# Kernel optimization log

Measured on AMD Instinct MI355X. Metric: run time of the kernel, lower is better.

The kernel has to match this reference:

```python
import jax, jax.numpy as jnp
import numpy as np

N_HEAD = 8

def setup_inputs() -> dict:
    key = jax.random.key(0)
    ks = jax.random.split(key, 5)
    B, T, C = 2, 4096, 512
    x = jax.random.normal(ks[0], (B, T, C), dtype=jnp.float32)
    w_attn = jax.random.normal(ks[1], (3 * C, C), dtype=jnp.float32) * (1.0 / np.sqrt(C))
    b_attn = jax.random.normal(ks[2], (3 * C,), dtype=jnp.float32) * 0.02
    w_proj = jax.random.normal(ks[3], (C, C), dtype=jnp.float32) * (1.0 / np.sqrt(C))
    b_proj = jax.random.normal(ks[4], (C,), dtype=jnp.float32) * 0.02
    return {"x": x, "w_attn": w_attn, "b_attn": b_attn, "w_proj": w_proj, "b_proj": b_proj}

def reference(x, w_attn, b_attn, w_proj, b_proj):
    B, T, C = x.shape
    H = N_HEAD
    D = C // H  # head dim
    qkv = x @ w_attn.T + b_attn  # [B,T,3C]
    q, k, v = jnp.split(qkv, 3, axis=-1)
    # b t (h d) -> b h t d
    def to_heads(t):
        return t.reshape(B, T, H, D).transpose(0, 2, 1, 3)
    q, k, v = to_heads(q), to_heads(k), to_heads(v)
    scale = 1.0 / np.sqrt(D).astype(np.float32)
    att = jnp.einsum('bhqd,bhkd->bhqk', q, k) * scale  # [B,H,T,T]
    causal = jnp.tril(jnp.ones((T, T), dtype=bool))
    att = jnp.where(causal[None, None], att, jnp.float32(-jnp.inf))
    att = jax.nn.softmax(att, axis=-1)
    y = jnp.einsum('bhqk,bhkd->bhqd', att, v)  # [B,H,T,D]
    y = y.transpose(0, 2, 1, 3).reshape(B, T, C)
    return y @ w_proj.T + b_proj
```

## Files before the change

kernel.cpp:

```cpp
#include <hip/hip_runtime.h>

typedef __attribute__((ext_vector_type(8))) __bf16 bf16x8;
typedef __attribute__((ext_vector_type(4))) __bf16 bf16x4;
typedef __attribute__((ext_vector_type(4))) float f32x4;
typedef __attribute__((ext_vector_type(16))) float f32x16;
typedef __attribute__((ext_vector_type(4))) unsigned uint32x4;

#define AS1 __attribute__((address_space(1)))
#define AS3 __attribute__((address_space(3)))

#if __has_builtin(__builtin_amdgcn_exp2f)
#define EXP2(x) __builtin_amdgcn_exp2f(x)
#else
#define EXP2(x) exp2f(x)
#endif

#define QSCALE 0.18033688011112042f

#define N_X 4194304
#define N_WA 786432
#define N_WP 262144
__global__ __launch_bounds__(256) void convert_all_k(const float* __restrict__ x,
                                                     const float* __restrict__ wa,
                                                     const float* __restrict__ wp,
                                                     __bf16* __restrict__ xb,
                                                     __bf16* __restrict__ wab,
                                                     __bf16* __restrict__ wpb) {
  int i = (blockIdx.x * 256 + threadIdx.x) * 4;
  const float* src;
  __bf16* dst;
  int off;
  if (i < N_X)              { src = x;  dst = xb;  off = i; }
  else if (i < N_X + N_WA)  { src = wa; dst = wab; off = i - N_X; }
  else if (i < N_X + N_WA + N_WP) { src = wp; dst = wpb; off = i - N_X - N_WA; }
  else return;
  float4 v = *reinterpret_cast<const float4*>(src + off);
  bf16x4 o;
  o[0] = (__bf16)v.x; o[1] = (__bf16)v.y; o[2] = (__bf16)v.z; o[3] = (__bf16)v.w;
  *reinterpret_cast<bf16x4*>(dst + off) = o;
}

template <int EPI>
__global__ __launch_bounds__(256) void gemm_bt(const __bf16* __restrict__ A,
                                               const __bf16* __restrict__ Bm,
                                               const float* __restrict__ bias,
                                               void* __restrict__ outp,
                                               __bf16* __restrict__ vtout,
                                               int M, int N, int K) {
  __shared__ __bf16 a_lds[128 * 64];
  __shared__ __bf16 b_lds[128 * 64];
  const int tid = threadIdx.x;
  const int lane = tid & 63;
  const int w = tid >> 6;
  const int wm = w >> 1, wn = w & 1;
  const int ll = lane & 15, lh = lane >> 4;
  const int m0 = blockIdx.y * 128;
  const int n0 = blockIdx.x * 128;
  f32x4 acc[4][4] = {};

  for (int k0 = 0; k0 < K; k0 += 64) {
    __syncthreads();
#pragma unroll
    for (int i = 0; i < 4; ++i) {
      int ch = i * 256 + w * 64 + lane;
      int r = ch >> 3, c8 = ch & 7;
      const __bf16* ga = A + (size_t)(m0 + r) * K + k0 + c8 * 8;
      __builtin_amdgcn_global_load_lds((const AS1 void*)ga,
                                       (AS3 void*)(a_lds + (i * 256 + w * 64) * 8), 16, 0, 0);
      const __bf16* gb = Bm + (size_t)(n0 + r) * K + k0 + c8 * 8;
      __builtin_amdgcn_global_load_lds((const AS1 void*)gb,
                                       (AS3 void*)(b_lds + (i * 256 + w * 64) * 8), 16, 0, 0);
    }
    __syncthreads();
#pragma unroll
    for (int kc = 0; kc < 2; ++kc) {
      bf16x8 af[4], bfr[4];
#pragma unroll
      for (int m = 0; m < 4; ++m)
        af[m] = *reinterpret_cast<const bf16x8*>(a_lds + (wm * 64 + m * 16 + ll) * 64 + kc * 32 + lh * 8);
#pragma unroll
      for (int n = 0; n < 4; ++n)
        bfr[n] = *reinterpret_cast<const bf16x8*>(b_lds + (wn * 64 + n * 16 + ll) * 64 + kc * 32 + lh * 8);
#pragma unroll
      for (int m = 0; m < 4; ++m)
#pragma unroll
        for (int n = 0; n < 4; ++n)
          acc[m][n] = __builtin_amdgcn_mfma_f32_16x16x32_bf16(af[m], bfr[n], acc[m][n], 0, 0, 0);
    }
  }
  if (EPI == 1) {
#pragma unroll
    for (int m = 0; m < 4; ++m) {
      int gm = m0 + wm * 64 + m * 16 + lh * 4;
#pragma unroll
      for (int n = 0; n < 4; ++n) {
        int gn = n0 + wn * 64 + n * 16 + ll;
        float bs = bias[gn];
#pragma unroll
        for (int r = 0; r < 4; ++r)
          ((float*)outp)[(size_t)(gm + r) * N + gn] = acc[m][n][r] + bs;
      }
    }
  } else if (n0 < 1024) {
    __syncthreads();
    __bf16* tb = (w < 2 ? a_lds : b_lds) + (w & 1) * 4096;
    const float sc = (n0 < 512) ? (float)QSCALE : 1.0f;
#pragma unroll
    for (int m = 0; m < 4; ++m)
#pragma unroll
      for (int n = 0; n < 4; ++n) {
        float bs = bias[n0 + wn * 64 + n * 16 + ll];
#pragma unroll
        for (int r = 0; r < 4; ++r)
          tb[(m * 16 + lh * 4 + r) * 64 + n * 16 + ll] = (__bf16)((acc[m][n][r] + bs) * sc);
      }
    const int rsub = lane >> 3, csub = (lane & 7) * 8;
#pragma unroll
    for (int i = 0; i < 8; ++i) {
      bf16x8 vv = *reinterpret_cast<const bf16x8*>(tb + (i * 8 + rsub) * 64 + csub);
      *reinterpret_cast<bf16x8*>((__bf16*)outp +
          (size_t)(m0 + wm * 64 + i * 8 + rsub) * N + n0 + wn * 64 + csub) = vv;
    }
  } else {
#pragma unroll
    for (int m = 0; m < 4; ++m) {
      int gm = m0 + wm * 64 + m * 16 + lh * 4;
#pragma unroll
      for (int n = 0; n < 4; ++n) {
        int gn = n0 + wn * 64 + n * 16 + ll;
        float bs = bias[gn];
        bf16x4 pk;
#pragma unroll
        for (int r = 0; r < 4; ++r) pk[r] = (__bf16)(acc[m][n][r] + bs);
        *reinterpret_cast<bf16x4*>(vtout + ((size_t)((gm >> 12) * 512 + (gn - 1024))) * 4096 + (gm & 4095)) = pk;
      }
    }
  }
}

struct Tbl { unsigned short t[204]; };
constexpr Tbl build_tbl() {
  Tbl T{};
  int sizes[204] = {};
  int n = 0;
  for (int p = 0; p < 2; ++p)
    for (int qx = 0; qx < 32; ++qx) {
      int total = 2 * qx + 2;
      int nch = (total + 11) / 12;
      int cum = 0;
      for (int q = 0; q < qx; ++q) cum += (2 * q + 13) / 12;
      for (int c = 0; c < nch; ++c) {
        int sz = total - 12 * c; if (sz > 12) sz = 12;
        T.t[n] = (unsigned short)(qx | (c << 5) | (p << 8) | ((cum + c) << 9));
        sizes[n] = sz;
        ++n;
      }
    }
  for (int i = 1; i < n; ++i) {
    unsigned short tv = T.t[i]; int sv = sizes[i];
    int j = i - 1;
    while (j >= 0 && sizes[j] < sv) { T.t[j + 1] = T.t[j]; sizes[j + 1] = sizes[j]; --j; }
    T.t[j + 1] = tv; sizes[j + 1] = sv;
  }
  return T;
}
__device__ __constant__ Tbl g_tbl = build_tbl();

__device__ inline unsigned cvtpk(float lo, float hi_) {
  unsigned r;
  asm("v_cvt_pk_bf16_f32 %0, %1, %2" : "=v"(r) : "v"(lo), "v"(hi_));
  return r;
}

__global__ __launch_bounds__(256, 4) void attn_k(const __bf16* __restrict__ qkv,
                                                 const __bf16* __restrict__ vt,
                                                 __bf16* __restrict__ opart,
                                                 float* __restrict__ lpart,
                                                 __bf16* __restrict__ y) {
  __shared__ __bf16 k_lds[2][64 * 64];
  __shared__ __bf16 v_lds[2][64 * 64];
  const int tid = threadIdx.x, lane = tid & 63, w = tid >> 6;
  const int hi = lane >> 5, q31 = lane & 31;
  const int swz = q31 & 7;

  const int bid = (int)blockIdx.x;
  const int e = g_tbl.t[bid >> 3];
  const int qx = e & 31, c = (e >> 5) & 7, p = (e >> 8) & 1, j = e >> 9;
  const int bh = (bid & 7) * 2 + p;
  const int pslot = bh * 102 + j;
  const int b = bh >> 3, h = bh & 7;
  const int q0 = qx * 128;
  const int qw0 = q0 + w * 32;
  const int t0 = 12 * c;
  const int t1 = min(12 * c + 12, 2 * qx + 2);

  const __bf16* qp = qkv + (size_t)b * 4096 * 1536 + h * 64;
  const __bf16* kp = qp + 512;
  const __bf16* vtp = vt + (size_t)(b * 512 + h * 64) * 4096;

  bf16x8 qf[4];
  {
    const __bf16* qr = qp + (size_t)(qw0 + q31) * 1536 + hi * 8;
#pragma unroll
    for (int d = 0; d < 4; ++d) qf[d] = *reinterpret_cast<const bf16x8*>(qr + d * 16);
  }

  f32x16 o0 = {}, o1 = {};
  float l_run = 0.f;

  auto stage = [&](int tt, int ss) {
    const int kv0s = tt * 64;
#pragma unroll
    for (int i = 0; i < 2; ++i) {
      int ch = i * 256 + tid;
      int r = ch >> 3, cc = ch & 7;
      int cs = cc ^ (r & 7);
      __builtin_amdgcn_global_load_lds(
          (const AS1 void*)(kp + (size_t)(kv0s + r) * 1536 + cs * 8),
          (AS3 void*)(&k_lds[ss][(i * 256 + w * 64) * 8]), 16, 0, 0);
      __builtin_amdgcn_global_load_lds(
          (const AS1 void*)(vtp + (size_t)r * 4096 + kv0s + cs * 8),
          (AS3 void*)(&v_lds[ss][(i * 256 + w * 64) * 8]), 16, 0, 0);
    }
  };

  stage(t0, 0);
  __builtin_amdgcn_sched_barrier(0);

  int slot = 0;
  for (int t = t0; t < t1; ++t) {
    asm volatile("s_waitcnt vmcnt(0)" ::: "memory");
    __builtin_amdgcn_sched_barrier(0);
    __builtin_amdgcn_s_barrier();
    __builtin_amdgcn_sched_barrier(0);
    if (t + 1 < t1) {
      stage(t + 1, slot ^ 1);
      __builtin_amdgcn_sched_barrier(0);
    }
    const int kv0 = t * 64;
    if (kv0 <= qw0 + 31) {
      f32x16 s0 = {}, s1 = {};
      __builtin_amdgcn_s_setprio(1);
#pragma unroll
      for (int d = 0; d < 4; ++d) {
        int c0 = ((d * 2 + hi) ^ swz) * 8;
        s0 = __builtin_amdgcn_mfma_f32_32x32x16_bf16(
            *reinterpret_cast<const bf16x8*>(&k_lds[slot][q31 * 64 + c0]), qf[d], s0, 0, 0, 0);
        s1 = __builtin_amdgcn_mfma_f32_32x32x16_bf16(
            *reinterpret_cast<const bf16x8*>(&k_lds[slot][(32 + q31) * 64 + c0]), qf[d], s1, 0, 0, 0);
      }
      __builtin_amdgcn_s_setprio(0);
      if (kv0 + 63 > qw0) {
        const int q = qw0 + q31;
#pragma unroll
        for (int r = 0; r < 16; ++r) {
          int crow = (r & 3) + 8 * (r >> 2) + 4 * hi;
          if (kv0 + crow > q) s0[r] = -1e30f;
          if (kv0 + 32 + crow > q) s1[r] = -1e30f;
        }
      }
#pragma unroll
      for (int r = 0; r < 16; ++r) s0[r] = EXP2(s0[r]);
#pragma unroll
      for (int r = 0; r < 16; ++r) s1[r] = EXP2(s1[r]);
      float a8[8];
#pragma unroll
      for (int r = 0; r < 8; ++r)
        a8[r] = (s0[r] + s0[r + 8]) + (s1[r] + s1[r + 8]);
#pragma unroll
      for (int st = 4; st >= 1; st >>= 1)
#pragma unroll
        for (int r = 0; r < 4; ++r)
          if (r < st) a8[r] += a8[r + st];
      l_run += a8[0] + __shfl_xor(a8[0], 32);
      uint32x4 pa[4];
#pragma unroll
      for (int half = 0; half < 2; ++half) {
        const int bse = half * 8;
        {
          unsigned x1 = cvtpk(s0[bse + 0], s0[bse + 1]);
          unsigned y1 = cvtpk(s0[bse + 4], s0[bse + 5]);
          asm("v_permlane32_swap_b32 %0, %1" : "+v"(x1), "+v"(y1));
          pa[half][0] = x1; pa[half][2] = y1;
          unsigned x2 = cvtpk(s0[bse + 2], s0[bse + 3]);
          unsigned y2 = cvtpk(s0[bse + 6], s0[bse + 7]);
          asm("v_permlane32_swap_b32 %0, %1" : "+v"(x2), "+v"(y2));
          pa[half][1] = x2; pa[half][3] = y2;
        }
        {
          unsigned x1 = cvtpk(s1[bse + 0], s1[bse + 1]);
          unsigned y1 = cvtpk(s1[bse + 4], s1[bse + 5]);
          asm("v_permlane32_swap_b32 %0, %1" : "+v"(x1), "+v"(y1));
          pa[2 + half][0] = x1; pa[2 + half][2] = y1;
          unsigned x2 = cvtpk(s1[bse + 2], s1[bse + 3]);
          unsigned y2 = cvtpk(s1[bse + 6], s1[bse + 7]);
          asm("v_permlane32_swap_b32 %0, %1" : "+v"(x2), "+v"(y2));
          pa[2 + half][1] = x2; pa[2 + half][3] = y2;
        }
      }
      __builtin_amdgcn_s_setprio(1);
#pragma unroll
      for (int ks = 0; ks < 4; ++ks) {
        int c0 = ((ks * 2 + hi) ^ swz) * 8;
        bf16x8 pfrag = __builtin_bit_cast(bf16x8, pa[ks]);
        o0 = __builtin_amdgcn_mfma_f32_32x32x16_bf16(
            *reinterpret_cast<const bf16x8*>(&v_lds[slot][q31 * 64 + c0]), pfrag, o0, 0, 0, 0);
        o1 = __builtin_amdgcn_mfma_f32_32x32x16_bf16(
            *reinterpret_cast<const bf16x8*>(&v_lds[slot][(32 + q31) * 64 + c0]), pfrag, o1, 0, 0, 0);
      }
      __builtin_amdgcn_s_setprio(0);
    }
    __builtin_amdgcn_sched_barrier(0);
    slot ^= 1;
  }

  const float inv = 1.f / l_run;
  const int rloc = w * 32 + q31;
  if (t0 == 0 && t1 == 2 * qx + 2) {
    __bf16* yr = y + ((size_t)b * 4096 + qw0 + q31) * 512 + h * 64;
#pragma unroll
    for (int g = 0; g < 4; ++g) {
      bf16x4 v0, v1;
#pragma unroll
      for (int jj = 0; jj < 4; ++jj) {
        v0[jj] = (__bf16)(o0[g * 4 + jj] * inv);
        v1[jj] = (__bf16)(o1[g * 4 + jj] * inv);
      }
      *reinterpret_cast<bf16x4*>(yr + 8 * g + 4 * hi) = v0;
      *reinterpret_cast<bf16x4*>(yr + 32 + 8 * g + 4 * hi) = v1;
    }
  } else {
    __bf16* ob = opart + ((size_t)pslot * 128 + rloc) * 64;
#pragma unroll
    for (int g = 0; g < 4; ++g) {
      bf16x4 v0, v1;
#pragma unroll
      for (int jj = 0; jj < 4; ++jj) {
        v0[jj] = (__bf16)(o0[g * 4 + jj] * inv);
        v1[jj] = (__bf16)(o1[g * 4 + jj] * inv);
      }
      *reinterpret_cast<bf16x4*>(ob + 8 * g + 4 * hi) = v0;
      *reinterpret_cast<bf16x4*>(ob + 32 + 8 * g + 4 * hi) = v1;
    }
    if (hi == 0) lpart[pslot * 128 + rloc] = l_run;
  }
}

__global__ __launch_bounds__(256) void combine_k(const __bf16* __restrict__ opart,
                                                 const float* __restrict__ lpart,
                                                 __bf16* __restrict__ y) {
  const int bid = (int)blockIdx.x;
  const int bh = bid >> 5, qx = bid & 31;
  if (qx < 6) return;
  const int b = bh >> 3, h = bh & 7;
  const int n = (2 * qx + 13) / 12;
  int cum = 0;
  for (int q = 0; q < qx; ++q) cum += (2 * q + 13) / 12;
  const int g0 = bh * 102 + cum;
  const int tid = threadIdx.x;
  const int r = tid >> 1, dh = (tid & 1) * 32;

  float W = 0.f;
  float acc[32] = {};
  for (int i = 0; i < n; ++i) {
    float wi = lpart[(g0 + i) * 128 + r];
    W += wi;
    const __bf16* op = opart + ((size_t)(g0 + i) * 128 + r) * 64 + dh;
#pragma unroll
    for (int jj = 0; jj < 4; ++jj) {
      bf16x8 v = *reinterpret_cast<const bf16x8*>(op + jj * 8);
#pragma unroll
      for (int e = 0; e < 8; ++e) acc[jj * 8 + e] += wi * (float)v[e];
    }
  }
  const float inv = 1.f / W;
  __bf16* yr = y + ((size_t)b * 4096 + qx * 128 + r) * 512 + h * 64 + dh;
#pragma unroll
  for (int jj = 0; jj < 4; ++jj) {
    bf16x8 ov;
#pragma unroll
    for (int e = 0; e < 8; ++e) ov[e] = (__bf16)(acc[jj * 8 + e] * inv);
    *reinterpret_cast<bf16x8*>(yr + jj * 8) = ov;
  }
}

extern "C" void kernel_launch(void* const* d_in, const int* in_sizes, int n_in,
                              void* d_out, int out_size, void* d_ws, size_t ws_size,
                              hipStream_t stream) {
  const float* x      = (const float*)d_in[0];
  const float* w_attn = (const float*)d_in[1];
  const float* b_attn = (const float*)d_in[2];
  const float* w_proj = (const float*)d_in[3];
  const float* b_proj = (const float*)d_in[4];
  float* out = (float*)d_out;

  const int Bv = 2, T = 4096, C = 512;
  const int M = Bv * T;

  const size_t NPART = (size_t)1632 * 128 * 64;
  __bf16* opart  = (__bf16*)d_ws;
  __bf16* x_bf   = opart;
  __bf16* wa_bf  = opart + NPART;
  __bf16* wp_bf  = wa_bf + (size_t)786432;
  __bf16* qkv_bf = wp_bf + (size_t)262144;
  __bf16* y_bf   = qkv_bf + (size_t)12582912;
  __bf16* vt_bf  = y_bf + (size_t)4194304;
  float*  lpart  = (float*)(vt_bf + (size_t)4194304);

  const int ntot = N_X + N_WA + N_WP;
  convert_all_k<<<(ntot / 4 + 255) / 256, 256, 0, stream>>>(x, w_attn, w_proj, x_bf, wa_bf, wp_bf);

  gemm_bt<0><<<dim3(3 * C / 128, M / 128), 256, 0, stream>>>(x_bf, wa_bf, b_attn, qkv_bf, vt_bf, M, 3 * C, C);
  attn_k<<<dim3(1632), 256, 0, stream>>>(qkv_bf, vt_bf, opart, lpart, y_bf);
  combine_k<<<dim3(512), 256, 0, stream>>>(opart, lpart, y_bf);
  gemm_bt<1><<<dim3(C / 128, M / 128), 256, 0, stream>>>(y_bf, wp_bf, b_proj, out, nullptr, M, C, C);
}
```

Measured before the change: 116.6 us.

## Remap GEMM blocks per XCD, split attention tile into halves, raise occupancy

The GEMM launches move to a 1D grid, with block indices remapped so each XCD handles a contiguous band of M rows, aiming for better L2 reuse. The attention kernel processes the two 32-row KV halves one after the other instead of together, which cuts live score registers so launch bounds can ask for 5 waves per SIMD. It also precomputes the global staging pointers and swizzled LDS column offsets, and defers the cross-lane row-sum reduction to the end of the loop. Partial outputs are now stored unnormalized, so combine_k only sums them and divides by the total, dropping per-partial weighting. The risks are higher register pressure or spilling at the tighter occupancy, and bf16 rounding of unnormalized partials.

```diff
diff --git a/kernel.cpp b/kernel.cpp
--- a/kernel.cpp
+++ b/kernel.cpp
@@ -54,8 +54,11 @@
   const int w = tid >> 6;
   const int wm = w >> 1, wn = w & 1;
   const int ll = lane & 15, lh = lane >> 4;
-  const int m0 = blockIdx.y * 128;
-  const int n0 = blockIdx.x * 128;
+  const int bid = (int)blockIdx.x;
+  const int NT = N >> 7;
+  const int xcd = bid & 7, lidx = bid >> 3;
+  const int m0 = (xcd * 8 + lidx / NT) * 128;
+  const int n0 = (lidx % NT) * 128;
   f32x4 acc[4][4] = {};
 
   for (int k0 = 0; k0 < K; k0 += 64) {
@@ -172,7 +175,7 @@
   return r;
 }
 
-__global__ __launch_bounds__(256, 4) void attn_k(const __bf16* __restrict__ qkv,
+__global__ __launch_bounds__(256, 5) void attn_k(const __bf16* __restrict__ qkv,
                                                  const __bf16* __restrict__ vt,
                                                  __bf16* __restrict__ opart,
                                                  float* __restrict__ lpart,
@@ -195,8 +198,12 @@
   const int t1 = min(12 * c + 12, 2 * qx + 2);
 
   const __bf16* qp = qkv + (size_t)b * 4096 * 1536 + h * 64;
-  const __bf16* kp = qp + 512;
   const __bf16* vtp = vt + (size_t)(b * 512 + h * 64) * 4096;
+
+  const int rr = tid >> 3;
+  const int csx = (tid & 7) ^ (rr & 7);
+  const __bf16* kg = qp + 512 + (size_t)(t0 * 64 + rr) * 1536 + csx * 8;
+  const __bf16* vg = vtp + (size_t)rr * 4096 + t0 * 64 + csx * 8;
 
   bf16x8 qf[4];
   {
@@ -205,26 +212,28 @@
     for (int d = 0; d < 4; ++d) qf[d] = *reinterpret_cast<const bf16x8*>(qr + d * 16);
   }
 
+  int co[4];
+#pragma unroll
+  for (int d = 0; d < 4; ++d) co[d] = (((d * 2 + hi) ^ swz) << 3);
+  const int rA = q31 * 64, rB = rA + 32 * 64;
+
   f32x16 o0 = {}, o1 = {};
   float l_run = 0.f;
 
-  auto stage = [&](int tt, int ss) {
-    const int kv0s = tt * 64;
-#pragma unroll
-    for (int i = 0; i < 2; ++i) {
-      int ch = i * 256 + tid;
-      int r = ch >> 3, cc = ch & 7;
-      int cs = cc ^ (r & 7);
-      __builtin_amdgcn_global_load_lds(
-          (const AS1 void*)(kp + (size_t)(kv0s + r) * 1536 + cs * 8),
-          (AS3 void*)(&k_lds[ss][(i * 256 + w * 64) * 8]), 16, 0, 0);
-      __builtin_amdgcn_global_load_lds(
-          (const AS1 void*)(vtp + (size_t)r * 4096 + kv0s + cs * 8),
-          (AS3 void*)(&v_lds[ss][(i * 256 + w * 64) * 8]), 16, 0, 0);
-    }
+  auto stage = [&](int ss) {
+    __builtin_amdgcn_global_load_lds((const AS1 void*)kg,
+        (AS3 void*)(&k_lds[ss][w * 512]), 16, 0, 0);
+    __builtin_amdgcn_global_load_lds((const AS1 void*)(kg + 32 * 1536),
+        (AS3 void*)(&k_lds[ss][2048 + w * 512]), 16, 0, 0);
+    __builtin_amdgcn_global_load_lds((const AS1 void*)vg,
+        (AS3 void*)(&v_lds[ss][w * 512]), 16, 0, 0);
+    __builtin_amdgcn_global_load_lds((const AS1 void*)(vg + 32 * 4096),
+        (AS3 void*)(&v_lds[ss][2048 + w * 512]), 16, 0, 0);
+    kg += 64 * 1536;
+    vg += 64;
   };
 
-  stage(t0, 0);
+  stage(0);
   __builtin_amdgcn_sched_barrier(0);
 
   int slot = 0;
@@ -234,89 +243,83 @@
     __builtin_amdgcn_s_barrier();
     __builtin_amdgcn_sched_barrier(0);
     if (t + 1 < t1) {
-      stage(t + 1, slot ^ 1);
+      stage(slot ^ 1);
       __builtin_amdgcn_sched_barrier(0);
     }
     const int kv0 = t * 64;
     if (kv0 <= qw0 + 31) {
-      f32x16 s0 = {}, s1 = {};
-      __builtin_amdgcn_s_setprio(1);
-#pragma unroll
-      for (int d = 0; d < 4; ++d) {
-        int c0 = ((d * 2 + hi) ^ swz) * 8;
-        s0 = __builtin_amdgcn_mfma_f32_32x32x16_bf16(
-            *reinterpret_cast<const bf16x8*>(&k_lds[slot][q31 * 64 + c0]), qf[d], s0, 0, 0, 0);
-        s1 = __builtin_amdgcn_mfma_f32_32x32x16_bf16(
-            *reinterpret_cast<const bf16x8*>(&k_lds[slot][(32 + q31) * 64 + c0]), qf[d], s1, 0, 0, 0);
-      }
-      __builtin_amdgcn_s_setprio(0);
-      if (kv0 + 63 > qw0) {
-        const int q = qw0 + q31;
-#pragma unroll
-        for (int r = 0; r < 16; ++r) {
-          int crow = (r & 3) + 8 * (r >> 2) + 4 * hi;
-          if (kv0 + crow > q) s0[r] = -1e30f;
-          if (kv0 + 32 + crow > q) s1[r] = -1e30f;
+      const __bf16* kb = &k_lds[slot][0];
+      const __bf16* vb = &v_lds[slot][0];
+      const int q = qw0 + q31;
+#pragma unroll
+      for (int half = 0; half < 2; ++half) {
+        const int rK = half ? rB : rA;
+        const int kvh = kv0 + half * 32;
+        f32x16 s = {};
+        __builtin_amdgcn_s_setprio(1);
+#pragma unroll
+        for (int d = 0; d < 4; ++d)
+          s = __builtin_amdgcn_mfma_f32_32x32x16_bf16(
+              *reinterpret_cast<const bf16x8*>(kb + rK + co[d]), qf[d], s, 0, 0, 0);
+        __builtin_amdgcn_s_setprio(0);
+        if (kvh + 31 > qw0) {
+#pragma unroll
+          for (int r = 0; r < 16; ++r) {
+            int crow = (r & 3) + 8 * (r >> 2) + 4 * hi;
+            if (kvh + crow > q) s[r] = -1e30f;
+          }
         }
-      }
-#pragma unroll
-      for (int r = 0; r < 16; ++r) s0[r] = EXP2(s0[r]);
-#pragma unroll
-      for (int r = 0; r < 16; ++r) s1[r] = EXP2(s1[r]);
-      float a8[8];
-#pragma unroll
-      for (int r = 0; r < 8; ++r)
-        a8[r] = (s0[r] + s0[r + 8]) + (s1[r] + s1[r + 8]);
-#pragma unroll
-      for (int st = 4; st >= 1; st >>= 1)
-#pragma unroll
-        for (int r = 0; r < 4; ++r)
-          if (r < st) a8[r] += a8[r + st];
-      l_run += a8[0] + __shfl_xor(a8[0], 32);
-      uint32x4 pa[4];
-#pragma unroll
-      for (int half = 0; half < 2; ++half) {
-        const int bse = half * 8;
+#pragma unroll
+        for (int r = 0; r < 16; ++r) s[r] = EXP2(s[r]);
         {
-          unsigned x1 = cvtpk(s0[bse + 0], s0[bse + 1]);
-          unsigned y1 = cvtpk(s0[bse + 4], s0[bse + 5]);
+          float u[8];
+#pragma unroll
+          for (int r = 0; r < 8; ++r) u[r] = s[r] + s[r + 8];
+          l_run += ((u[0] + u[1]) + (u[2] + u[3])) + ((u[4] + u[5]) + (u[6] + u[7]));
+        }
+        uint32x4 pa0, pa1;
+        {
+          unsigned x1 = cvtpk(s[0], s[1]);
+          unsigned y1 = cvtpk(s[4], s[5]);
           asm("v_permlane32_swap_b32 %0, %1" : "+v"(x1), "+v"(y1));
-          pa[half][0] = x1; pa[half][2] = y1;
-          unsigned x2 = cvtpk(s0[bse + 2], s0[bse + 3]);
-          unsigned y2 = cvtpk(s0[bse + 6], s0[bse + 7]);
+          pa0[0] = x1; pa0[2] = y1;
+          unsigned x2 = cvtpk(s[2], s[3]);
+          unsigned y2 = cvtpk(s[6], s[7]);
           asm("v_permlane32_swap_b32 %0, %1" : "+v"(x2), "+v"(y2));
-          pa[half][1] = x2; pa[half][3] = y2;
+          pa0[1] = x2; pa0[3] = y2;
+          x1 = cvtpk(s[8], s[9]);
+          y1 = cvtpk(s[12], s[13]);
+          asm("v_permlane32_swap_b32 %0, %1" : "+v"(x1), "+v"(y1));
+          pa1[0] = x1; pa1[2] = y1;
+          x2 = cvtpk(s[10], s[11]);
+          y2 = cvtpk(s[14], s[15]);
+          asm("v_permlane32_swap_b32 %0, %1" : "+v"(x2), "+v"(y2));
+          pa1[1] = x2; pa1[3] = y2;
         }
-        {
-          unsigned x1 = cvtpk(s1[bse + 0], s1[bse + 1]);
-          unsigned y1 = cvtpk(s1[bse + 4], s1[bse + 5]);
-          asm("v_permlane32_swap_b32 %0, %1" : "+v"(x1), "+v"(y1));
-          pa[2 + half][0] = x1; pa[2 + half][2] = y1;
-          unsigned x2 = cvtpk(s1[bse + 2], s1[bse + 3]);
-          unsigned y2 = cvtpk(s1[bse + 6], s1[bse + 7]);
-          asm("v_permlane32_swap_b32 %0, %1" : "+v"(x2), "+v"(y2));
-          pa[2 + half][1] = x2; pa[2 + half][3] = y2;
-        }
-      }
-      __builtin_amdgcn_s_setprio(1);
-#pragma unroll
-      for (int ks = 0; ks < 4; ++ks) {
-        int c0 = ((ks * 2 + hi) ^ swz) * 8;
-        bf16x8 pfrag = __builtin_bit_cast(bf16x8, pa[ks]);
+        const int ks0 = half * 2;
+        bf16x8 pf0 = __builtin_bit_cast(bf16x8, pa0);
+        bf16x8 pf1 = __builtin_bit_cast(bf16x8, pa1);
+        __builtin_amdgcn_s_setprio(1);
         o0 = __builtin_amdgcn_mfma_f32_32x32x16_bf16(
-            *reinterpret_cast<const bf16x8*>(&v_lds[slot][q31 * 64 + c0]), pfrag, o0, 0, 0, 0);
+            *reinterpret_cast<const bf16x8*>(vb + rA + co[ks0]), pf0, o0, 0, 0, 0);
         o1 = __builtin_amdgcn_mfma_f32_32x32x16_bf16(
-            *reinterpret_cast<const bf16x8*>(&v_lds[slot][(32 + q31) * 64 + c0]), pfrag, o1, 0, 0, 0);
-      }
-      __builtin_amdgcn_s_setprio(0);
+            *reinterpret_cast<const bf16x8*>(vb + rB + co[ks0]), pf0, o1, 0, 0, 0);
+        o0 = __builtin_amdgcn_mfma_f32_32x32x16_bf16(
+            *reinterpret_cast<const bf16x8*>(vb + rA + co[ks0 + 1]), pf1, o0, 0, 0, 0);
+        o1 = __builtin_amdgcn_mfma_f32_32x32x16_bf16(
+            *reinterpret_cast<const bf16x8*>(vb + rB + co[ks0 + 1]), pf1, o1, 0, 0, 0);
+        __builtin_amdgcn_s_setprio(0);
+      }
     }
     __builtin_amdgcn_sched_barrier(0);
     slot ^= 1;
   }
 
-  const float inv = 1.f / l_run;
+  l_run += __shfl_xor(l_run, 32);
+
   const int rloc = w * 32 + q31;
   if (t0 == 0 && t1 == 2 * qx + 2) {
+    const float inv = 1.f / l_run;
     __bf16* yr = y + ((size_t)b * 4096 + qw0 + q31) * 512 + h * 64;
 #pragma unroll
     for (int g = 0; g < 4; ++g) {
@@ -336,8 +339,8 @@
       bf16x4 v0, v1;
 #pragma unroll
       for (int jj = 0; jj < 4; ++jj) {
-        v0[jj] = (__bf16)(o0[g * 4 + jj] * inv);
-        v1[jj] = (__bf16)(o1[g * 4 + jj] * inv);
+        v0[jj] = (__bf16)(o0[g * 4 + jj]);
+        v1[jj] = (__bf16)(o1[g * 4 + jj]);
       }
       *reinterpret_cast<bf16x4*>(ob + 8 * g + 4 * hi) = v0;
       *reinterpret_cast<bf16x4*>(ob + 32 + 8 * g + 4 * hi) = v1;
@@ -363,14 +366,13 @@
   float W = 0.f;
   float acc[32] = {};
   for (int i = 0; i < n; ++i) {
-    float wi = lpart[(g0 + i) * 128 + r];
-    W += wi;
+    W += lpart[(g0 + i) * 128 + r];
     const __bf16* op = opart + ((size_t)(g0 + i) * 128 + r) * 64 + dh;
 #pragma unroll
     for (int jj = 0; jj < 4; ++jj) {
       bf16x8 v = *reinterpret_cast<const bf16x8*>(op + jj * 8);
 #pragma unroll
-      for (int e = 0; e < 8; ++e) acc[jj * 8 + e] += wi * (float)v[e];
+      for (int e = 0; e < 8; ++e) acc[jj * 8 + e] += (float)v[e];
     }
   }
   const float inv = 1.f / W;
@@ -410,8 +412,8 @@
   const int ntot = N_X + N_WA + N_WP;
   convert_all_k<<<(ntot / 4 + 255) / 256, 256, 0, stream>>>(x, w_attn, w_proj, x_bf, wa_bf, wp_bf);
 
-  gemm_bt<0><<<dim3(3 * C / 128, M / 128), 256, 0, stream>>>(x_bf, wa_bf, b_attn, qkv_bf, vt_bf, M, 3 * C, C);
+  gemm_bt<0><<<dim3((3 * C / 128) * (M / 128)), 256, 0, stream>>>(x_bf, wa_bf, b_attn, qkv_bf, vt_bf, M, 3 * C, C);
   attn_k<<<dim3(1632), 256, 0, stream>>>(qkv_bf, vt_bf, opart, lpart, y_bf);
   combine_k<<<dim3(512), 256, 0, stream>>>(opart, lpart, y_bf);
-  gemm_bt<1><<<dim3(C / 128, M / 128), 256, 0, stream>>>(y_bf, wp_bf, b_proj, out, nullptr, M, C, C);
-}
+  gemm_bt<1><<<dim3((C / 128) * (M / 128)), 256, 0, stream>>>(y_bf, wp_bf, b_proj, out, nullptr, M, C, C);
+}
```

Result: slower. 152.5 us (+30.8%).

## Remap GEMM blocks per XCD and defer softmax row-sum reduction

Applied to the files above, without the earlier changes.

GEMM launches switch to a 1D grid and remap block ids so that each of the 8 XCDs handles a contiguous band of M rows, which should improve L2 reuse of A tiles. The attention kernel replaces the per-iteration cross-lane shuffle for the softmax denominator with a per-lane sum that is reduced once after the loop. Partial outputs are stored unnormalized, so the combine kernel simply sums them and divides by the total l. This removes per-tile shuffles and some multiplies, but unnormalized partials stored in bf16 can have larger magnitude and lose some relative precision.

```diff
diff --git a/kernel.cpp b/kernel.cpp
--- a/kernel.cpp
+++ b/kernel.cpp
@@ -54,8 +54,11 @@
   const int w = tid >> 6;
   const int wm = w >> 1, wn = w & 1;
   const int ll = lane & 15, lh = lane >> 4;
-  const int m0 = blockIdx.y * 128;
-  const int n0 = blockIdx.x * 128;
+  const int bid = (int)blockIdx.x;
+  const int NT = N >> 7;
+  const int xcd = bid & 7, lidx = bid >> 3;
+  const int m0 = (xcd * 8 + lidx / NT) * 128;
+  const int n0 = (lidx % NT) * 128;
   f32x4 acc[4][4] = {};
 
   for (int k0 = 0; k0 < K; k0 += 64) {
@@ -263,16 +266,13 @@
       for (int r = 0; r < 16; ++r) s0[r] = EXP2(s0[r]);
 #pragma unroll
       for (int r = 0; r < 16; ++r) s1[r] = EXP2(s1[r]);
-      float a8[8];
-#pragma unroll
-      for (int r = 0; r < 8; ++r)
-        a8[r] = (s0[r] + s0[r + 8]) + (s1[r] + s1[r + 8]);
-#pragma unroll
-      for (int st = 4; st >= 1; st >>= 1)
-#pragma unroll
-        for (int r = 0; r < 4; ++r)
-          if (r < st) a8[r] += a8[r + st];
-      l_run += a8[0] + __shfl_xor(a8[0], 32);
+      {
+        float a8[8];
+#pragma unroll
+        for (int r = 0; r < 8; ++r)
+          a8[r] = (s0[r] + s0[r + 8]) + (s1[r] + s1[r + 8]);
+        l_run += (((a8[0] + a8[1]) + (a8[2] + a8[3])) + ((a8[4] + a8[5]) + (a8[6] + a8[7])));
+      }
       uint32x4 pa[4];
 #pragma unroll
       for (int half = 0; half < 2; ++half) {
@@ -314,9 +314,11 @@
     slot ^= 1;
   }
 
-  const float inv = 1.f / l_run;
+  l_run += __shfl_xor(l_run, 32);
+
   const int rloc = w * 32 + q31;
   if (t0 == 0 && t1 == 2 * qx + 2) {
+    const float inv = 1.f / l_run;
     __bf16* yr = y + ((size_t)b * 4096 + qw0 + q31) * 512 + h * 64;
 #pragma unroll
     for (int g = 0; g < 4; ++g) {
@@ -336,8 +338,8 @@
       bf16x4 v0, v1;
 #pragma unroll
       for (int jj = 0; jj < 4; ++jj) {
-        v0[jj] = (__bf16)(o0[g * 4 + jj] * inv);
-        v1[jj] = (__bf16)(o1[g * 4 + jj] * inv);
+        v0[jj] = (__bf16)(o0[g * 4 + jj]);
+        v1[jj] = (__bf16)(o1[g * 4 + jj]);
       }
       *reinterpret_cast<bf16x4*>(ob + 8 * g + 4 * hi) = v0;
       *reinterpret_cast<bf16x4*>(ob + 32 + 8 * g + 4 * hi) = v1;
@@ -363,14 +365,13 @@
   float W = 0.f;
   float acc[32] = {};
   for (int i = 0; i < n; ++i) {
-    float wi = lpart[(g0 + i) * 128 + r];
-    W += wi;
+    W += lpart[(g0 + i) * 128 + r];
     const __bf16* op = opart + ((size_t)(g0 + i) * 128 + r) * 64 + dh;
 #pragma unroll
     for (int jj = 0; jj < 4; ++jj) {
       bf16x8 v = *reinterpret_cast<const bf16x8*>(op + jj * 8);
 #pragma unroll
-      for (int e = 0; e < 8; ++e) acc[jj * 8 + e] += wi * (float)v[e];
+      for (int e = 0; e < 8; ++e) acc[jj * 8 + e] += (float)v[e];
     }
   }
   const float inv = 1.f / W;
@@ -410,8 +411,8 @@
   const int ntot = N_X + N_WA + N_WP;
   convert_all_k<<<(ntot / 4 + 255) / 256, 256, 0, stream>>>(x, w_attn, w_proj, x_bf, wa_bf, wp_bf);
 
-  gemm_bt<0><<<dim3(3 * C / 128, M / 128), 256, 0, stream>>>(x_bf, wa_bf, b_attn, qkv_bf, vt_bf, M, 3 * C, C);
+  gemm_bt<0><<<dim3((3 * C / 128) * (M / 128)), 256, 0, stream>>>(x_bf, wa_bf, b_attn, qkv_bf, vt_bf, M, 3 * C, C);
   attn_k<<<dim3(1632), 256, 0, stream>>>(qkv_bf, vt_bf, opart, lpart, y_bf);
   combine_k<<<dim3(512), 256, 0, stream>>>(opart, lpart, y_bf);
-  gemm_bt<1><<<dim3(C / 128, M / 128), 256, 0, stream>>>(y_bf, wp_bf, b_proj, out, nullptr, M, C, C);
-}
+  gemm_bt<1><<<dim3((C / 128) * (M / 128)), 256, 0, stream>>>(y_bf, wp_bf, b_proj, out, nullptr, M, C, C);
+}
```

Measured after the change: 113.0 us. 3.1% less time.
